# Performance work log

Measured on AMD Instinct MI355X. Metric: run time of the kernel, lower is better.

Reference implementation:

```python
import jax, jax.numpy as jnp
import numpy as np

N_NODES = 200000
N_EDGES = 3200000
F_IN = 16
N_CLASSES = 16


def setup_inputs() -> dict:
    key = jax.random.key(0)
    ks = jax.random.split(key, 8)
    s = 1.0 / np.sqrt(F_IN)
    return {
        "x": jax.random.normal(ks[0], (N_NODES, F_IN), dtype=jnp.float32),
        "edge_index": jax.random.randint(ks[1], (2, N_EDGES), 0, N_NODES, dtype=jnp.int32),
        "eps1": jnp.zeros((), dtype=jnp.float32),
        "w1a": jax.random.normal(ks[2], (F_IN, 16), dtype=jnp.float32) * s,
        "b1a": jnp.zeros((16,), dtype=jnp.float32),
        "w1b": jax.random.normal(ks[3], (16, 16), dtype=jnp.float32) * 0.25,
        "b1b": jnp.zeros((16,), dtype=jnp.float32),
        "eps2": jnp.zeros((), dtype=jnp.float32),
        "w2a": jax.random.normal(ks[4], (16, N_CLASSES), dtype=jnp.float32) * 0.25,
        "b2a": jnp.zeros((N_CLASSES,), dtype=jnp.float32),
        "w2b": jax.random.normal(ks[5], (N_CLASSES, N_CLASSES), dtype=jnp.float32) * 0.25,
        "b2b": jnp.zeros((N_CLASSES,), dtype=jnp.float32),
    }


def _gin_conv(x, src, dst, eps, wa, ba, wb, bb, n_nodes):
    # sum aggregation of source-node features into destination nodes
    agg = jax.ops.segment_sum(x[src], dst, num_segments=n_nodes)  # [N, F]
    h = (1.0 + eps) * x + agg
    # 2-layer MLP: Linear -> ReLU -> Linear
    h = jax.nn.relu(h @ wa + ba) @ wb + bb
    return h


def reference(x, edge_index, eps1, w1a, b1a, w1b, b1b, eps2, w2a, b2a, w2b, b2b):
    src, dst = edge_index[0], edge_index[1]
    n = x.shape[0]
    h = jax.nn.relu(_gin_conv(x, src, dst, eps1, w1a, b1a, w1b, b1b, n))
    # F.dropout with training=False is identity (module assumed in eval mode)
    h = _gin_conv(h, src, dst, eps2, w2a, b2a, w2b, b2b, n)
    return jax.nn.log_softmax(h, axis=1)
```

## Files before the change

kernel.cpp:

```cpp
#include <hip/hip_runtime.h>

#define N_NODES 200000
#define N_EDGES 3200000
#define F 16
#define NB 782
#define NB_PAD 832
#define HIST_EPB 8192
#define HIST_BLOCKS ((N_EDGES + HIST_EPB - 1) / HIST_EPB)
#define HIST_T 1024
#define PART_EPB 8192
#define PART_BLOCKS ((N_EDGES + PART_EPB - 1) / PART_EPB)
#define PART_T 1024
#define CAP 5120
#define GIN_NODES 64
#define GIN_BLOCKS ((N_NODES + GIN_NODES - 1) / GIN_NODES)


__device__ __forceinline__ unsigned bf16pack2(float lo, float hi) {
    unsigned ul = __float_as_uint(lo);
    unsigned uh = __float_as_uint(hi);
    ul = (ul + 0x7fffu + ((ul >> 16) & 1u)) >> 16;
    uh = (uh + 0x7fffu + ((uh >> 16) & 1u)) >> 16;
    return ul | (uh << 16);
}
#define BLO(w) __uint_as_float((w) << 16)
#define BHI(w) __uint_as_float((w) & 0xffff0000u)

__device__ __forceinline__ void gacc(const unsigned short* __restrict__ xin,
                                     int s, float acc[16]) {
    const uint4* r = (const uint4*)(xin + (size_t)s * F);
    uint4 w0 = r[0], w1 = r[1];
    acc[0]  += BLO(w0.x); acc[1]  += BHI(w0.x);
    acc[2]  += BLO(w0.y); acc[3]  += BHI(w0.y);
    acc[4]  += BLO(w0.z); acc[5]  += BHI(w0.z);
    acc[6]  += BLO(w0.w); acc[7]  += BHI(w0.w);
    acc[8]  += BLO(w1.x); acc[9]  += BHI(w1.x);
    acc[10] += BLO(w1.y); acc[11] += BHI(w1.y);
    acc[12] += BLO(w1.z); acc[13] += BHI(w1.z);
    acc[14] += BLO(w1.w); acc[15] += BHI(w1.w);
}


__global__ __launch_bounds__(256) void conv_bf16(const float* __restrict__ x,
                                                 unsigned* __restrict__ xb) {
    int i = blockIdx.x * blockDim.x + threadIdx.x;
    if (i >= N_NODES * F / 8) return;
    const float4* p = (const float4*)(x + (size_t)i * 8);
    float4 a = p[0], b = p[1];
    uint4 r;
    r.x = bf16pack2(a.x, a.y);
    r.y = bf16pack2(a.z, a.w);
    r.z = bf16pack2(b.x, b.y);
    r.w = bf16pack2(b.z, b.w);
    ((uint4*)xb)[i] = r;
}


__global__ __launch_bounds__(HIST_T) void bucket_hist(const int* __restrict__ dst,
                                                      int* __restrict__ bcnt) {
    __shared__ int lh[NB];
    const int t = threadIdx.x;
    for (int i = t; i < NB; i += HIST_T) lh[i] = 0;
    __syncthreads();

    const int base4 = blockIdx.x * (HIST_EPB / 4);
    #pragma unroll
    for (int k = 0; k < HIST_EPB / 4 / HIST_T; ++k) {
        int i4 = base4 + k * HIST_T + t;
        if (i4 < N_EDGES / 4) {
            int4 d = *(const int4*)(dst + i4 * 4);
            atomicAdd(&lh[d.x >> 8], 1);
            atomicAdd(&lh[d.y >> 8], 1);
            atomicAdd(&lh[d.z >> 8], 1);
            atomicAdd(&lh[d.w >> 8], 1);
        }
    }
    __syncthreads();
    for (int i = t; i < NB; i += HIST_T) {
        int v = lh[i];
        if (v) atomicAdd(&bcnt[i], v);
    }
}


__global__ __launch_bounds__(1024) void bucket_scan(const int* __restrict__ bcnt,
                                                    int* __restrict__ bbase,
                                                    int* __restrict__ bcursor) {
    __shared__ int part[1024];
    const int t = threadIdx.x;
    int v = (t < NB) ? bcnt[t] : 0;
    part[t] = v;
    __syncthreads();
    for (int off = 1; off < 1024; off <<= 1) {
        int other = (t >= off) ? part[t - off] : 0;
        __syncthreads();
        part[t] += other;
        __syncthreads();
    }
    if (t < NB) {
        int ex = part[t] - v;
        bbase[t] = ex;
        bcursor[t] = ex;
    }
    if (t == 1023) bbase[NB] = part[1023];
}


__global__ __launch_bounds__(PART_T) void partition_ms(const int* __restrict__ src,
                                                       const int* __restrict__ dst,
                                                       int* __restrict__ bcursor,
                                                       int* __restrict__ ebuf) {
    __shared__ int lh[NB];
    __shared__ int gbase[NB];
    const int t = threadIdx.x;
    for (int i = t; i < NB; i += PART_T) lh[i] = 0;
    __syncthreads();

    const int base4 = blockIdx.x * (PART_EPB / 4);
    #pragma unroll
    for (int k = 0; k < PART_EPB / 4 / PART_T; ++k) {
        int i4 = base4 + k * PART_T + t;
        if (i4 < N_EDGES / 4) {
            int4 d = *(const int4*)(dst + i4 * 4);
            atomicAdd(&lh[d.x >> 8], 1);
            atomicAdd(&lh[d.y >> 8], 1);
            atomicAdd(&lh[d.z >> 8], 1);
            atomicAdd(&lh[d.w >> 8], 1);
        }
    }
    __syncthreads();
    for (int i = t; i < NB; i += PART_T) {
        int c = lh[i];
        gbase[i] = c ? atomicAdd(&bcursor[i], c) : 0;
        lh[i] = 0;
    }
    __syncthreads();
    #pragma unroll
    for (int k = 0; k < PART_EPB / 4 / PART_T; ++k) {
        int i4 = base4 + k * PART_T + t;
        if (i4 < N_EDGES / 4) {
            int4 s = *(const int4*)(src + i4 * 4);
            int4 d = *(const int4*)(dst + i4 * 4);
            int b, p;
            b = d.x >> 8; p = atomicAdd(&lh[b], 1); ebuf[gbase[b] + p] = (s.x << 8) | (d.x & 255);
            b = d.y >> 8; p = atomicAdd(&lh[b], 1); ebuf[gbase[b] + p] = (s.y << 8) | (d.y & 255);
            b = d.z >> 8; p = atomicAdd(&lh[b], 1); ebuf[gbase[b] + p] = (s.z << 8) | (d.z & 255);
            b = d.w >> 8; p = atomicAdd(&lh[b], 1); ebuf[gbase[b] + p] = (s.w << 8) | (d.w & 255);
        }
    }
}


__global__ __launch_bounds__(256) void sort_csr(const int* __restrict__ bbase,
                                                int* __restrict__ ebuf,
                                                int* __restrict__ noffs,
                                                int* __restrict__ scratch) {
    __shared__ int srec[CAP];
    __shared__ int hist[256];
    __shared__ int lofs[256];
    const int t = threadIdx.x;
    const int b = blockIdx.x;
    hist[t] = 0;
    __syncthreads();

    const int beg = bbase[b];
    const int end = bbase[b + 1];
    const int sz = end - beg;
    const int n = b * 256 + t;

    for (int k = beg + t; k < end; k += 256)
        atomicAdd(&hist[ebuf[k] & 255], 1);
    __syncthreads();
    int v = hist[t];
    lofs[t] = v;
    __syncthreads();
    for (int off = 1; off < 256; off <<= 1) {
        int o = (t >= off) ? lofs[t - off] : 0;
        __syncthreads();
        lofs[t] += o;
        __syncthreads();
    }
    const int myend = lofs[t];
    const int mybeg = myend - v;
    __syncthreads();
    hist[t] = mybeg;
    __syncthreads();

    if (sz <= CAP) {
        for (int k = beg + t; k < end; k += 256) {
            int rec = ebuf[k];
            int p = atomicAdd(&hist[rec & 255], 1);
            srec[p] = rec >> 8;
        }
        __syncthreads();
        for (int k = t; k < sz; k += 256) ebuf[beg + k] = srec[k];
    } else {
        for (int k = beg + t; k < end; k += 256) scratch[k] = ebuf[k];
        __syncthreads();
        for (int k = beg + t; k < end; k += 256) {
            int rec = scratch[k];
            int p = atomicAdd(&hist[rec & 255], 1);
            ebuf[beg + p] = rec >> 8;
        }
    }

    if (n < N_NODES) noffs[n] = beg + mybeg;
    if (b == 0 && t == 0) noffs[N_NODES] = N_EDGES;
}


template <bool LAYER2>
__global__ __launch_bounds__(256) void gin_gather(
    const unsigned short* __restrict__ xin,
    const int* __restrict__ noffs,
    const int* __restrict__ ebuf,
    const float* __restrict__ epsp,
    const float* __restrict__ wa, const float* __restrict__ ba,
    const float* __restrict__ wb, const float* __restrict__ bb,
    void* __restrict__ outp) {
    __shared__ float swa[256], swb[256], sba[16], sbb[16];
    const int t = threadIdx.x;
    swa[t] = wa[t];
    swb[t] = wb[t];
    if (t < 16) { sba[t] = ba[t]; sbb[t] = bb[t]; }
    __syncthreads();

    const int n = blockIdx.x * GIN_NODES + (t >> 2);
    const int sub = t & 3;
    if (n >= N_NODES) return;

    const int beg = noffs[n];
    const int end = noffs[n + 1];

    float acc[16];
    #pragma unroll
    for (int q = 0; q < 16; ++q) acc[q] = 0.0f;

    int k = beg + sub;
    for (; k + 4 < end; k += 8) {
        int s0 = ebuf[k];
        int s1 = ebuf[k + 4];
        gacc(xin, s0, acc);
        gacc(xin, s1, acc);
    }
    if (k < end) gacc(xin, ebuf[k], acc);

    #pragma unroll
    for (int q = 0; q < 16; ++q) {
        acc[q] += __shfl_xor(acc[q], 1);
        acc[q] += __shfl_xor(acc[q], 2);
    }
    if (sub != 0) return;

    const float eps = 1.0f + *epsp;
    const uint4* xr = (const uint4*)(xin + (size_t)n * F);
    uint4 w0 = xr[0], w1 = xr[1];
    float h[16];
    h[0]  = fmaf(eps, BLO(w0.x), acc[0]);   h[1]  = fmaf(eps, BHI(w0.x), acc[1]);
    h[2]  = fmaf(eps, BLO(w0.y), acc[2]);   h[3]  = fmaf(eps, BHI(w0.y), acc[3]);
    h[4]  = fmaf(eps, BLO(w0.z), acc[4]);   h[5]  = fmaf(eps, BHI(w0.z), acc[5]);
    h[6]  = fmaf(eps, BLO(w0.w), acc[6]);   h[7]  = fmaf(eps, BHI(w0.w), acc[7]);
    h[8]  = fmaf(eps, BLO(w1.x), acc[8]);   h[9]  = fmaf(eps, BHI(w1.x), acc[9]);
    h[10] = fmaf(eps, BLO(w1.y), acc[10]);  h[11] = fmaf(eps, BHI(w1.y), acc[11]);
    h[12] = fmaf(eps, BLO(w1.z), acc[12]);  h[13] = fmaf(eps, BHI(w1.z), acc[13]);
    h[14] = fmaf(eps, BLO(w1.w), acc[14]);  h[15] = fmaf(eps, BHI(w1.w), acc[15]);

    float m[16];
    #pragma unroll
    for (int jj = 0; jj < 16; ++jj) {
        float a = sba[jj];
        #pragma unroll
        for (int i = 0; i < 16; ++i) a = fmaf(h[i], swa[i * 16 + jj], a);
        m[jj] = fmaxf(a, 0.0f);
    }

    float o[16];
    #pragma unroll
    for (int jj = 0; jj < 16; ++jj) {
        float a = sbb[jj];
        #pragma unroll
        for (int i = 0; i < 16; ++i) a = fmaf(m[i], swb[i * 16 + jj], a);
        o[jj] = LAYER2 ? a : fmaxf(a, 0.0f);
    }

    if (LAYER2) {
        float mx = o[0];
        #pragma unroll
        for (int jj = 1; jj < 16; ++jj) mx = fmaxf(mx, o[jj]);
        float s = 0.0f;
        #pragma unroll
        for (int jj = 0; jj < 16; ++jj) s += expf(o[jj] - mx);
        float lse = mx + logf(s);
        float* orow = (float*)outp + (size_t)n * F;
        #pragma unroll
        for (int q = 0; q < 4; ++q) {
            ((float4*)orow)[q] = make_float4(o[q * 4 + 0] - lse, o[q * 4 + 1] - lse,
                                             o[q * 4 + 2] - lse, o[q * 4 + 3] - lse);
        }
    } else {
        unsigned* orow = (unsigned*)outp + (size_t)n * 8;
        uint4 r0, r1;
        r0.x = bf16pack2(o[0],  o[1]);   r0.y = bf16pack2(o[2],  o[3]);
        r0.z = bf16pack2(o[4],  o[5]);   r0.w = bf16pack2(o[6],  o[7]);
        r1.x = bf16pack2(o[8],  o[9]);   r1.y = bf16pack2(o[10], o[11]);
        r1.z = bf16pack2(o[12], o[13]);  r1.w = bf16pack2(o[14], o[15]);
        ((uint4*)orow)[0] = r0;
        ((uint4*)orow)[1] = r1;
    }
}


__global__ __launch_bounds__(256) void scatter_kernel(
    const float* __restrict__ feat,
    const int* __restrict__ src,
    const int* __restrict__ dst,
    float* __restrict__ agg) {
    int e = blockIdx.x * blockDim.x + threadIdx.x;
    if (e >= N_EDGES) return;
    int s = src[e];
    int d = dst[e];
    const float4* fs = (const float4*)(feat + (size_t)s * F);
    float* ad = agg + (size_t)d * F;
    #pragma unroll
    for (int q = 0; q < 4; ++q) {
        float4 v = fs[q];
        atomicAdd(ad + q * 4 + 0, v.x);
        atomicAdd(ad + q * 4 + 1, v.y);
        atomicAdd(ad + q * 4 + 2, v.z);
        atomicAdd(ad + q * 4 + 3, v.w);
    }
}

template <bool RELU_OUT, bool LOGSOFTMAX>
__global__ __launch_bounds__(256) void mlp_kernel(
    const float* __restrict__ xin,
    const float* __restrict__ agg,
    const float* __restrict__ epsp,
    const float* __restrict__ wa, const float* __restrict__ ba,
    const float* __restrict__ wb, const float* __restrict__ bb,
    float* __restrict__ out) {
    __shared__ float swa[256], swb[256], sba[16], sbb[16];
    int t = threadIdx.x;
    swa[t] = wa[t];
    swb[t] = wb[t];
    if (t < 16) { sba[t] = ba[t]; sbb[t] = bb[t]; }
    __syncthreads();

    int n = blockIdx.x * blockDim.x + t;
    if (n >= N_NODES) return;

    float eps = 1.0f + *epsp;
    const float4* xr = (const float4*)(xin + (size_t)n * F);
    const float4* ar = (const float4*)(agg + (size_t)n * F);
    float h[16];
    #pragma unroll
    for (int q = 0; q < 4; ++q) {
        float4 xv = xr[q];
        float4 av = ar[q];
        h[q * 4 + 0] = fmaf(eps, xv.x, av.x);
        h[q * 4 + 1] = fmaf(eps, xv.y, av.y);
        h[q * 4 + 2] = fmaf(eps, xv.z, av.z);
        h[q * 4 + 3] = fmaf(eps, xv.w, av.w);
    }

    float m[16];
    #pragma unroll
    for (int jj = 0; jj < 16; ++jj) {
        float a = sba[jj];
        #pragma unroll
        for (int i = 0; i < 16; ++i) a = fmaf(h[i], swa[i * 16 + jj], a);
        m[jj] = fmaxf(a, 0.0f);
    }

    float o[16];
    #pragma unroll
    for (int jj = 0; jj < 16; ++jj) {
        float a = sbb[jj];
        #pragma unroll
        for (int i = 0; i < 16; ++i) a = fmaf(m[i], swb[i * 16 + jj], a);
        o[jj] = RELU_OUT ? fmaxf(a, 0.0f) : a;
    }

    if (LOGSOFTMAX) {
        float mx = o[0];
        #pragma unroll
        for (int jj = 1; jj < 16; ++jj) mx = fmaxf(mx, o[jj]);
        float s = 0.0f;
        #pragma unroll
        for (int jj = 0; jj < 16; ++jj) s += expf(o[jj] - mx);
        float lse = mx + logf(s);
        #pragma unroll
        for (int jj = 0; jj < 16; ++jj) o[jj] -= lse;
    }

    float4* orow = (float4*)(out + (size_t)n * F);
    #pragma unroll
    for (int q = 0; q < 4; ++q) {
        orow[q] = make_float4(o[q * 4 + 0], o[q * 4 + 1], o[q * 4 + 2], o[q * 4 + 3]);
    }
}


extern "C" void kernel_launch(void* const* d_in, const int* in_sizes, int n_in,
                              void* d_out, int out_size, void* d_ws, size_t ws_size,
                              hipStream_t stream) {
    const float* x    = (const float*)d_in[0];
    const int*   ei   = (const int*)d_in[1];
    const float* eps1 = (const float*)d_in[2];
    const float* w1a  = (const float*)d_in[3];
    const float* b1a  = (const float*)d_in[4];
    const float* w1b  = (const float*)d_in[5];
    const float* b1b  = (const float*)d_in[6];
    const float* eps2 = (const float*)d_in[7];
    const float* w2a  = (const float*)d_in[8];
    const float* b2a  = (const float*)d_in[9];
    const float* w2b  = (const float*)d_in[10];
    const float* b2b  = (const float*)d_in[11];

    float* out = (float*)d_out;
    const int* src = ei;
    const int* dst = ei + N_EDGES;

    size_t off_bcnt    = 0;
    size_t off_bbase   = off_bcnt + (size_t)NB_PAD * 4;
    size_t off_bcursor = off_bbase + (size_t)NB_PAD * 4;
    size_t off_noffs   = off_bcursor + (size_t)NB_PAD * 4;
    size_t off_ebuf    = off_noffs + ((size_t)N_NODES + 64) * 4;
    size_t off_xb      = off_ebuf + (size_t)N_EDGES * 4;
    size_t off_hb      = off_xb + (size_t)N_NODES * F * 2;
    size_t need        = off_hb + (size_t)N_NODES * F * 2;

    if (ws_size >= need) {
        int*            bcnt    = (int*)((char*)d_ws + off_bcnt);
        int*            bbase   = (int*)((char*)d_ws + off_bbase);
        int*            bcursor = (int*)((char*)d_ws + off_bcursor);
        int*            noffs   = (int*)((char*)d_ws + off_noffs);
        int*            ebuf    = (int*)((char*)d_ws + off_ebuf);
        unsigned short* xb      = (unsigned short*)((char*)d_ws + off_xb);
        unsigned short* hb      = (unsigned short*)((char*)d_ws + off_hb);

        hipMemsetAsync(bcnt, 0, (size_t)NB * 4, stream);
        bucket_hist<<<HIST_BLOCKS, HIST_T, 0, stream>>>(dst, bcnt);
        conv_bf16<<<(N_NODES * F / 8 + 255) / 256, 256, 0, stream>>>(x, (unsigned*)xb);
        bucket_scan<<<1, 1024, 0, stream>>>(bcnt, bbase, bcursor);
        partition_ms<<<PART_BLOCKS, PART_T, 0, stream>>>(src, dst, bcursor, ebuf);
        sort_csr<<<NB, 256, 0, stream>>>(bbase, ebuf, noffs, (int*)d_out);

        gin_gather<false><<<GIN_BLOCKS, 256, 0, stream>>>(
            xb, noffs, ebuf, eps1, w1a, b1a, w1b, b1b, hb);
        gin_gather<true><<<GIN_BLOCKS, 256, 0, stream>>>(
            hb, noffs, ebuf, eps2, w2a, b2a, w2b, b2b, out);
    } else {
        float* agg = (float*)d_ws;
        const int edge_blocks = (N_EDGES + 255) / 256;
        const int node_blocks = (N_NODES + 255) / 256;
        const size_t agg_bytes = (size_t)N_NODES * F * sizeof(float);

        hipMemsetAsync(agg, 0, agg_bytes, stream);
        scatter_kernel<<<edge_blocks, 256, 0, stream>>>(x, src, dst, agg);
        mlp_kernel<true, false><<<node_blocks, 256, 0, stream>>>(
            x, agg, eps1, w1a, b1a, w1b, b1b, out);

        hipMemsetAsync(agg, 0, agg_bytes, stream);
        scatter_kernel<<<edge_blocks, 256, 0, stream>>>(out, src, dst, agg);
        mlp_kernel<false, true><<<node_blocks, 256, 0, stream>>>(
            out, agg, eps2, w2a, b2a, w2b, b2b, out);
    }
}
```

Before: 159.3 us.

## Store per-block bucket histograms and column-scan them instead of recounting in partition

The first pass now writes each edge block's bucket histogram to a count matrix, and a new column-scan kernel turns it into per-block exclusive offsets. The partition kernel can then skip its own histogram pass and its global atomic cursor claims, and the partition becomes deterministic. The gather loop is also unrolled to four outstanding row loads per thread to raise memory-level parallelism. This adds a kernel launch, a count-matrix buffer (391x832 ints) and more registers in the gather kernel.

New measurement: 148.6 us. 6.7% less time.

```diff
diff --git a/kernel.cpp b/kernel.cpp
--- a/kernel.cpp
+++ b/kernel.cpp
@@ -5,12 +5,9 @@
 #define F 16
 #define NB 782
 #define NB_PAD 832
-#define HIST_EPB 8192
-#define HIST_BLOCKS ((N_EDGES + HIST_EPB - 1) / HIST_EPB)
-#define HIST_T 1024
-#define PART_EPB 8192
-#define PART_BLOCKS ((N_EDGES + PART_EPB - 1) / PART_EPB)
-#define PART_T 1024
+#define EPB 8192
+#define EBLOCKS ((N_EDGES + EPB - 1) / EPB)
+#define ET 1024
 #define CAP 5120
 #define GIN_NODES 64
 #define GIN_BLOCKS ((N_NODES + GIN_NODES - 1) / GIN_NODES)
@@ -26,10 +23,7 @@
 #define BLO(w) __uint_as_float((w) << 16)
 #define BHI(w) __uint_as_float((w) & 0xffff0000u)
 
-__device__ __forceinline__ void gacc(const unsigned short* __restrict__ xin,
-                                     int s, float acc[16]) {
-    const uint4* r = (const uint4*)(xin + (size_t)s * F);
-    uint4 w0 = r[0], w1 = r[1];
+__device__ __forceinline__ void acc8(uint4 w0, uint4 w1, float acc[16]) {
     acc[0]  += BLO(w0.x); acc[1]  += BHI(w0.x);
     acc[2]  += BLO(w0.y); acc[3]  += BHI(w0.y);
     acc[4]  += BLO(w0.z); acc[5]  += BHI(w0.z);
@@ -56,17 +50,17 @@
 }
 
 
-__global__ __launch_bounds__(HIST_T) void bucket_hist(const int* __restrict__ dst,
-                                                      int* __restrict__ bcnt) {
+__global__ __launch_bounds__(ET) void count_kernel(const int* __restrict__ dst,
+                                                   int* __restrict__ cntmat) {
     __shared__ int lh[NB];
     const int t = threadIdx.x;
-    for (int i = t; i < NB; i += HIST_T) lh[i] = 0;
-    __syncthreads();
-
-    const int base4 = blockIdx.x * (HIST_EPB / 4);
-    #pragma unroll
-    for (int k = 0; k < HIST_EPB / 4 / HIST_T; ++k) {
-        int i4 = base4 + k * HIST_T + t;
+    for (int i = t; i < NB; i += ET) lh[i] = 0;
+    __syncthreads();
+
+    const int base4 = blockIdx.x * (EPB / 4);
+    #pragma unroll
+    for (int k = 0; k < EPB / 4 / ET; ++k) {
+        int i4 = base4 + k * ET + t;
         if (i4 < N_EDGES / 4) {
             int4 d = *(const int4*)(dst + i4 * 4);
             atomicAdd(&lh[d.x >> 8], 1);
@@ -76,16 +70,33 @@
         }
     }
     __syncthreads();
-    for (int i = t; i < NB; i += HIST_T) {
-        int v = lh[i];
-        if (v) atomicAdd(&bcnt[i], v);
-    }
+    int* row = cntmat + (size_t)blockIdx.x * NB_PAD;
+    for (int i = t; i < NB; i += ET) row[i] = lh[i];
+}
+
+
+__global__ __launch_bounds__(512) void colscan(int* __restrict__ cntmat,
+                                               int* __restrict__ bcnt) {
+    __shared__ int part[512];
+    const int t = threadIdx.x;
+    const int b = blockIdx.x;
+    int v = 0;
+    if (t < EBLOCKS) v = cntmat[(size_t)t * NB_PAD + b];
+    part[t] = v;
+    __syncthreads();
+    for (int off = 1; off < 512; off <<= 1) {
+        int o = (t >= off) ? part[t - off] : 0;
+        __syncthreads();
+        part[t] += o;
+        __syncthreads();
+    }
+    if (t < EBLOCKS) cntmat[(size_t)t * NB_PAD + b] = part[t] - v;
+    if (t == EBLOCKS - 1) bcnt[b] = part[t];
 }
 
 
 __global__ __launch_bounds__(1024) void bucket_scan(const int* __restrict__ bcnt,
-                                                    int* __restrict__ bbase,
-                                                    int* __restrict__ bcursor) {
+                                                    int* __restrict__ bbase) {
     __shared__ int part[1024];
     const int t = threadIdx.x;
     int v = (t < NB) ? bcnt[t] : 0;
@@ -97,55 +108,38 @@
         part[t] += other;
         __syncthreads();
     }
-    if (t < NB) {
-        int ex = part[t] - v;
-        bbase[t] = ex;
-        bcursor[t] = ex;
-    }
+    if (t < NB) bbase[t] = part[t] - v;
     if (t == 1023) bbase[NB] = part[1023];
 }
 
 
-__global__ __launch_bounds__(PART_T) void partition_ms(const int* __restrict__ src,
-                                                       const int* __restrict__ dst,
-                                                       int* __restrict__ bcursor,
-                                                       int* __restrict__ ebuf) {
+__global__ __launch_bounds__(ET) void partition2(const int* __restrict__ src,
+                                                 const int* __restrict__ dst,
+                                                 const int* __restrict__ bbase,
+                                                 const int* __restrict__ cntmat,
+                                                 int* __restrict__ ebuf) {
     __shared__ int lh[NB];
-    __shared__ int gbase[NB];
-    const int t = threadIdx.x;
-    for (int i = t; i < NB; i += PART_T) lh[i] = 0;
-    __syncthreads();
-
-    const int base4 = blockIdx.x * (PART_EPB / 4);
-    #pragma unroll
-    for (int k = 0; k < PART_EPB / 4 / PART_T; ++k) {
-        int i4 = base4 + k * PART_T + t;
-        if (i4 < N_EDGES / 4) {
-            int4 d = *(const int4*)(dst + i4 * 4);
-            atomicAdd(&lh[d.x >> 8], 1);
-            atomicAdd(&lh[d.y >> 8], 1);
-            atomicAdd(&lh[d.z >> 8], 1);
-            atomicAdd(&lh[d.w >> 8], 1);
-        }
-    }
-    __syncthreads();
-    for (int i = t; i < NB; i += PART_T) {
-        int c = lh[i];
-        gbase[i] = c ? atomicAdd(&bcursor[i], c) : 0;
+    __shared__ int sbase[NB];
+    const int t = threadIdx.x;
+    const int* row = cntmat + (size_t)blockIdx.x * NB_PAD;
+    for (int i = t; i < NB; i += ET) {
+        sbase[i] = bbase[i] + row[i];
         lh[i] = 0;
     }
     __syncthreads();
-    #pragma unroll
-    for (int k = 0; k < PART_EPB / 4 / PART_T; ++k) {
-        int i4 = base4 + k * PART_T + t;
+
+    const int base4 = blockIdx.x * (EPB / 4);
+    #pragma unroll
+    for (int k = 0; k < EPB / 4 / ET; ++k) {
+        int i4 = base4 + k * ET + t;
         if (i4 < N_EDGES / 4) {
             int4 s = *(const int4*)(src + i4 * 4);
             int4 d = *(const int4*)(dst + i4 * 4);
             int b, p;
-            b = d.x >> 8; p = atomicAdd(&lh[b], 1); ebuf[gbase[b] + p] = (s.x << 8) | (d.x & 255);
-            b = d.y >> 8; p = atomicAdd(&lh[b], 1); ebuf[gbase[b] + p] = (s.y << 8) | (d.y & 255);
-            b = d.z >> 8; p = atomicAdd(&lh[b], 1); ebuf[gbase[b] + p] = (s.z << 8) | (d.z & 255);
-            b = d.w >> 8; p = atomicAdd(&lh[b], 1); ebuf[gbase[b] + p] = (s.w << 8) | (d.w & 255);
+            b = d.x >> 8; p = atomicAdd(&lh[b], 1); ebuf[sbase[b] + p] = (s.x << 8) | (d.x & 255);
+            b = d.y >> 8; p = atomicAdd(&lh[b], 1); ebuf[sbase[b] + p] = (s.y << 8) | (d.y & 255);
+            b = d.z >> 8; p = atomicAdd(&lh[b], 1); ebuf[sbase[b] + p] = (s.z << 8) | (d.z & 255);
+            b = d.w >> 8; p = atomicAdd(&lh[b], 1); ebuf[sbase[b] + p] = (s.w << 8) | (d.w & 255);
         }
     }
 }
@@ -237,13 +231,38 @@
     for (int q = 0; q < 16; ++q) acc[q] = 0.0f;
 
     int k = beg + sub;
+    for (; k + 12 < end; k += 16) {
+        int s0 = ebuf[k];
+        int s1 = ebuf[k + 4];
+        int s2 = ebuf[k + 8];
+        int s3 = ebuf[k + 12];
+        const uint4* r0 = (const uint4*)(xin + (size_t)s0 * F);
+        const uint4* r1 = (const uint4*)(xin + (size_t)s1 * F);
+        const uint4* r2 = (const uint4*)(xin + (size_t)s2 * F);
+        const uint4* r3 = (const uint4*)(xin + (size_t)s3 * F);
+        uint4 a0 = r0[0], a1 = r0[1];
+        uint4 b0 = r1[0], b1 = r1[1];
+        uint4 c0 = r2[0], c1 = r2[1];
+        uint4 d0 = r3[0], d1 = r3[1];
+        acc8(a0, a1, acc);
+        acc8(b0, b1, acc);
+        acc8(c0, c1, acc);
+        acc8(d0, d1, acc);
+    }
     for (; k + 4 < end; k += 8) {
         int s0 = ebuf[k];
         int s1 = ebuf[k + 4];
-        gacc(xin, s0, acc);
-        gacc(xin, s1, acc);
-    }
-    if (k < end) gacc(xin, ebuf[k], acc);
+        const uint4* r0 = (const uint4*)(xin + (size_t)s0 * F);
+        const uint4* r1 = (const uint4*)(xin + (size_t)s1 * F);
+        uint4 a0 = r0[0], a1 = r0[1];
+        uint4 b0 = r1[0], b1 = r1[1];
+        acc8(a0, a1, acc);
+        acc8(b0, b1, acc);
+    }
+    if (k < end) {
+        const uint4* r0 = (const uint4*)(xin + (size_t)ebuf[k] * F);
+        acc8(r0[0], r0[1], acc);
+    }
 
     #pragma unroll
     for (int q = 0; q < 16; ++q) {
@@ -421,29 +440,29 @@
     const int* src = ei;
     const int* dst = ei + N_EDGES;
 
-    size_t off_bcnt    = 0;
-    size_t off_bbase   = off_bcnt + (size_t)NB_PAD * 4;
-    size_t off_bcursor = off_bbase + (size_t)NB_PAD * 4;
-    size_t off_noffs   = off_bcursor + (size_t)NB_PAD * 4;
-    size_t off_ebuf    = off_noffs + ((size_t)N_NODES + 64) * 4;
-    size_t off_xb      = off_ebuf + (size_t)N_EDGES * 4;
-    size_t off_hb      = off_xb + (size_t)N_NODES * F * 2;
-    size_t need        = off_hb + (size_t)N_NODES * F * 2;
+    size_t off_bcnt   = 0;
+    size_t off_bbase  = off_bcnt + (size_t)NB_PAD * 4;
+    size_t off_noffs  = off_bbase + (size_t)NB_PAD * 4;
+    size_t off_ebuf   = off_noffs + ((size_t)N_NODES + 64) * 4;
+    size_t off_xb     = off_ebuf + (size_t)N_EDGES * 4;
+    size_t off_hb     = off_xb + (size_t)N_NODES * F * 2;
+    size_t off_cnt    = off_hb + (size_t)N_NODES * F * 2;
+    size_t need       = off_cnt + (size_t)EBLOCKS * NB_PAD * 4;
 
     if (ws_size >= need) {
-        int*            bcnt    = (int*)((char*)d_ws + off_bcnt);
-        int*            bbase   = (int*)((char*)d_ws + off_bbase);
-        int*            bcursor = (int*)((char*)d_ws + off_bcursor);
-        int*            noffs   = (int*)((char*)d_ws + off_noffs);
-        int*            ebuf    = (int*)((char*)d_ws + off_ebuf);
-        unsigned short* xb      = (unsigned short*)((char*)d_ws + off_xb);
-        unsigned short* hb      = (unsigned short*)((char*)d_ws + off_hb);
-
-        hipMemsetAsync(bcnt, 0, (size_t)NB * 4, stream);
-        bucket_hist<<<HIST_BLOCKS, HIST_T, 0, stream>>>(dst, bcnt);
+        int*            bcnt   = (int*)((char*)d_ws + off_bcnt);
+        int*            bbase  = (int*)((char*)d_ws + off_bbase);
+        int*            noffs  = (int*)((char*)d_ws + off_noffs);
+        int*            ebuf   = (int*)((char*)d_ws + off_ebuf);
+        unsigned short* xb     = (unsigned short*)((char*)d_ws + off_xb);
+        unsigned short* hb     = (unsigned short*)((char*)d_ws + off_hb);
+        int*            cntmat = (int*)((char*)d_ws + off_cnt);
+
+        count_kernel<<<EBLOCKS, ET, 0, stream>>>(dst, cntmat);
         conv_bf16<<<(N_NODES * F / 8 + 255) / 256, 256, 0, stream>>>(x, (unsigned*)xb);
-        bucket_scan<<<1, 1024, 0, stream>>>(bcnt, bbase, bcursor);
-        partition_ms<<<PART_BLOCKS, PART_T, 0, stream>>>(src, dst, bcursor, ebuf);
+        colscan<<<NB, 512, 0, stream>>>(cntmat, bcnt);
+        bucket_scan<<<1, 1024, 0, stream>>>(bcnt, bbase);
+        partition2<<<EBLOCKS, ET, 0, stream>>>(src, dst, bbase, cntmat, ebuf);
         sort_csr<<<NB, 256, 0, stream>>>(bbase, ebuf, noffs, (int*)d_out);
 
         gin_gather<false><<<GIN_BLOCKS, 256, 0, stream>>>(
```
